# Optimization experiments

Hardware: AMD Instinct MI355X
Metric: run time of the kernel (lower is better)

## Reference

```python
import jax, jax.numpy as jnp
import numpy as np

N = 10000      # nodes
E = 80000      # edges
D = 128        # d_model
H = 8          # num_heads
DH = 128       # d_head
DFF = 512      # d_ff
CLAMP = 5.0
EPS = 1e-5


def setup_inputs() -> dict:
    key = jax.random.key(0)
    ks = jax.random.split(key, 10)
    s = 0.05
    return {
        "feat": jax.random.normal(ks[0], (N, D), jnp.float32),
        "src": jax.random.randint(ks[1], (E,), 0, N),
        "dst": jax.random.randint(ks[2], (E,), 0, N),
        # projections stored as (in, out); x @ W == torch Linear(bias=False)
        "Wq": jax.random.normal(ks[3], (D, H * DH), jnp.float32) * s,
        "Wk": jax.random.normal(ks[4], (D, H * DH), jnp.float32) * s,
        "Wv": jax.random.normal(ks[5], (D, H * DH), jnp.float32) * s,
        "Wo": jax.random.normal(ks[6], (H * DH, D), jnp.float32) * s,
        "g1": jnp.ones((D,), jnp.float32),
        "b1": jnp.zeros((D,), jnp.float32),
        "W1": jax.random.normal(ks[7], (D, DFF), jnp.float32) * s,
        "bf1": jnp.zeros((DFF,), jnp.float32),
        "W2": jax.random.normal(ks[8], (DFF, D), jnp.float32) * s,
        "bf2": jnp.zeros((D,), jnp.float32),
        "g2": jnp.ones((D,), jnp.float32),
        "b2": jnp.zeros((D,), jnp.float32),
    }


def _layer_norm(x, g, b):
    mu = x.mean(-1, keepdims=True)
    xc = x - mu
    var = (xc * xc).mean(-1, keepdims=True)
    return xc * jax.lax.rsqrt(var + EPS) * g + b


def reference(feat, src, dst, Wq, Wk, Wv, Wo, g1, b1, W1, bf1, W2, bf2, g2, b2):
    h_src = feat[src]                              # (E, D) gather
    h_dst = feat[dst]                              # (E, D)
    q = (h_dst @ Wq).reshape(E, H, DH)             # query from destination node
    k = (h_src @ Wk).reshape(E, H, DH)
    v = (h_src @ Wv).reshape(E, H, DH)
    # per-edge logits: QK dot per head, scale, clamp
    u = jnp.clip((q * k).sum(-1) / np.sqrt(DH), -CLAMP, CLAMP)  # (E, H)
    # edge_softmax over incoming edges of each destination node
    m = jax.ops.segment_max(u, dst, num_segments=N)             # (N, H)
    ex = jnp.exp(u - m[dst])
    den = jax.ops.segment_sum(ex, dst, num_segments=N)          # (N, H)
    a = ex / den[dst]                                           # (E, H)
    # weighted V, segment-sum to destination nodes
    agg = jax.ops.segment_sum(a[..., None] * v, dst, num_segments=N)  # (N, H, DH)
    uh = _layer_norm(feat + agg.reshape(N, H * DH) @ Wo, g1, b1)
    ffn = jax.nn.relu(uh @ W1 + bf1) @ W2 + bf2
    return _layer_norm(uh + ffn, g2, b2)
```

## Files before the change

kernel.cpp:

```cpp
#include <hip/hip_runtime.h>

typedef unsigned int uint;
typedef unsigned short ushort;
typedef __attribute__((ext_vector_type(8))) short short8;
typedef __attribute__((ext_vector_type(4))) float f32x4;

#define DEV static __device__ __forceinline__

DEV float bf_lo(uint v) { return __uint_as_float(v << 16); }
DEV float bf_hi(uint v) { return __uint_as_float(v & 0xffff0000u); }
DEV ushort f2bf(float f) {
    uint u = __float_as_uint(f);
    u += 0x7fffu + ((u >> 16) & 1u);
    return (ushort)(u >> 16);
}
DEV void stC(float* p, float v) { *p = v; }
DEV void stC(ushort* p, float v) { *p = f2bf(v); }

#define DPPADD(v, ctrl) \
    ((v) + __int_as_float(__builtin_amdgcn_mov_dpp(__float_as_int(v), (ctrl), 0xF, 0xF, true)))

__global__ __launch_bounds__(256) void zero_kernel(int4* __restrict__ p, int n4)
{
    int i = blockIdx.x * 256 + threadIdx.x;
    if (i < n4) p[i] = int4{0, 0, 0, 0};
}

template <typename OT>
DEV void transp_body(float (*tile)[65], const float* __restrict__ in,
                     OT* __restrict__ out, int R, int C, int bid, int t)
{
    const int nbx = C >> 6;
    const int bx = bid % nbx, by = bid / nbx;
#pragma unroll
    for (int it = 0; it < 4; ++it) {
        int idx = it * 256 + t;
        int rr = idx >> 4, cc4 = (idx & 15) * 4;
        float4 v = *reinterpret_cast<const float4*>(in + (size_t)(by * 64 + rr) * C + bx * 64 + cc4);
        tile[cc4][rr] = v.x; tile[cc4 + 1][rr] = v.y;
        tile[cc4 + 2][rr] = v.z; tile[cc4 + 3][rr] = v.w;
    }
    __syncthreads();
#pragma unroll
    for (int it = 0; it < 4; ++it) {
        int idx = it * 256 + t;
        int cc = idx >> 4, rr4 = (idx & 15) * 4;
        OT* po = out + (size_t)(bx * 64 + cc) * R + by * 64 + rr4;
        if constexpr (__is_same(OT, float)) {
            float4 o = { tile[cc][rr4], tile[cc][rr4 + 1], tile[cc][rr4 + 2], tile[cc][rr4 + 3] };
            *reinterpret_cast<float4*>(po) = o;
        } else {
            ushort4 o = { f2bf(tile[cc][rr4]), f2bf(tile[cc][rr4 + 1]),
                          f2bf(tile[cc][rr4 + 2]), f2bf(tile[cc][rr4 + 3]) };
            *reinterpret_cast<ushort4*>(po) = o;
        }
    }
}

__global__ __launch_bounds__(256) void prep0_kernel(
    const float* __restrict__ feat, ushort* __restrict__ featbf,
    const float* __restrict__ Wo, float* __restrict__ WoT,
    const float* __restrict__ W1, ushort* __restrict__ W1T,
    const float* __restrict__ W2, ushort* __restrict__ W2T,
    const int* __restrict__ dst, int* __restrict__ cntd, int N, int E)
{
    __shared__ float tile[64][65];
    const int nf = (N * 32 + 255) / 256;
    const int b = blockIdx.x, t = threadIdx.x;
    if (b < nf) {
        int i = b * 256 + t;
        if (i >= N * 32) return;
        float4 v = reinterpret_cast<const float4*>(feat)[i];
        ushort4 o;
        o.x = f2bf(v.x); o.y = f2bf(v.y); o.z = f2bf(v.z); o.w = f2bf(v.w);
        reinterpret_cast<ushort4*>(featbf)[i] = o;
    } else if (b < nf + 32) {
        transp_body<float>(tile, Wo, WoT, 1024, 128, b - nf, t);
    } else if (b < nf + 48) {
        transp_body<ushort>(tile, W1, W1T, 128, 512, b - nf - 32, t);
    } else if (b < nf + 64) {
        transp_body<ushort>(tile, W2, W2T, 512, 128, b - nf - 48, t);
    } else {
        int e = (b - nf - 64) * 256 + t;
        if (e >= E) return;
        atomicAdd(&cntd[dst[e]], 1);
    }
}

__global__ __launch_bounds__(1024) void scan1_kernel(
    const int* __restrict__ cntd, int* __restrict__ offd, int* __restrict__ curd, int N)
{
    __shared__ int ls[1024];
    const int t = threadIdx.x;
    const int chunk = (N + 1023) >> 10;
    int base = t * chunk;
    int s = 0;
    for (int i = 0; i < chunk; ++i) {
        int idx = base + i;
        if (idx < N) s += cntd[idx];
    }
    ls[t] = s;
    __syncthreads();
    for (int d = 1; d < 1024; d <<= 1) {
        int v = (t >= d) ? ls[t - d] : 0;
        __syncthreads();
        ls[t] += v;
        __syncthreads();
    }
    int run = t ? ls[t - 1] : 0;
    for (int i = 0; i < chunk; ++i) {
        int idx = base + i;
        if (idx < N) {
            offd[idx] = run;
            curd[idx] = run;
            run += cntd[idx];
        }
    }
    if (t == 1023) offd[N] = run;
}

__global__ __launch_bounds__(256) void scat_mpt_kernel(
    const int* __restrict__ src, const int* __restrict__ dst,
    int* __restrict__ curd, int* __restrict__ src_d, int* __restrict__ dst_d, int E, int eb,
    const float* __restrict__ Wq, const float* __restrict__ Wk,
    const float* __restrict__ Wv, const float* __restrict__ WoT,
    ushort* __restrict__ MPT)
{
    __shared__ char lds[65536];
    const int b = blockIdx.x, t = threadIdx.x;
    if (b < eb) {
        int e = b * 256 + t;
        if (e >= E) return;
        int s = src[e], d = dst[e];
        int pd = atomicAdd(&curd[d], 1);
        src_d[pd] = s;
        dst_d[pd] = d;
        return;
    }
    char* As = lds;
    char* Bs = lds + 32768;

    const int mb = b - eb;
    const int part = mb >> 3, h = mb & 7;
    const int lane = t & 63, w = t >> 6;
    const int frow = lane & 15, kgrp = lane >> 4;

    const float* Asrc = part ? WoT : Wk;
    const float* Bsrc = part ? Wv : Wq;
    const float ascale = part ? 1.f : 0.08838834764831845f;

#pragma unroll
    for (int it = 0; it < 16; ++it) {
        int idx = it * 256 + t;
        int r = idx >> 5, c4 = (idx & 31) * 4;
        size_t goff = (size_t)r * 1024 + h * 128 + c4;
        float4 va = *reinterpret_cast<const float4*>(Asrc + goff);
        ushort4 ua = { f2bf(va.x * ascale), f2bf(va.y * ascale),
                       f2bf(va.z * ascale), f2bf(va.w * ascale) };
        *reinterpret_cast<ushort4*>(&As[r * 256 + ((c4 * 2) ^ ((r & 7) << 4))]) = ua;
        float4 vb = *reinterpret_cast<const float4*>(Bsrc + goff);
        ushort4 ub = { f2bf(vb.x), f2bf(vb.y), f2bf(vb.z), f2bf(vb.w) };
        *reinterpret_cast<ushort4*>(&Bs[r * 256 + ((c4 * 2) ^ ((r & 7) << 4))]) = ub;
    }
    __syncthreads();

    f32x4 acc[2][8] = {};
#pragma unroll
    for (int ks = 0; ks < 4; ++ks) {
        int koff = ks * 64 + kgrp * 16;
        short8 bfr[8];
#pragma unroll
        for (int fn = 0; fn < 8; ++fn) {
            int col = fn * 16 + frow;
            bfr[fn] = *reinterpret_cast<const short8*>(&Bs[col * 256 + (koff ^ ((col & 7) << 4))]);
        }
#pragma unroll
        for (int fm = 0; fm < 2; ++fm) {
            int row = w * 32 + fm * 16 + frow;
            short8 a = *reinterpret_cast<const short8*>(&As[row * 256 + (koff ^ ((row & 7) << 4))]);
#pragma unroll
            for (int fn = 0; fn < 8; ++fn)
                acc[fm][fn] = __builtin_amdgcn_mfma_f32_16x16x32_bf16(a, bfr[fn], acc[fm][fn], 0, 0, 0);
        }
    }

    const size_t base = ((size_t)part * 1024 + h * 128) * 128;
#pragma unroll
    for (int fm = 0; fm < 2; ++fm)
#pragma unroll
        for (int fn = 0; fn < 8; ++fn)
#pragma unroll
            for (int r = 0; r < 4; ++r) {
                int j = w * 32 + fm * 16 + kgrp * 4 + r;
                int i = fn * 16 + frow;
                MPT[base + (size_t)j * 128 + i] = f2bf(acc[fm][fn][r]);
            }
}

template <int NTILE, typename OT, bool BIAS, bool RELU>
__global__ __launch_bounds__(256) void gemm_k128(
    const ushort* __restrict__ A, const ushort* __restrict__ BT,
    const float* __restrict__ bias,
    OT* __restrict__ C, int M, int NC)
{
    constexpr int FN = NTILE * 2;
    constexpr int WN = NTILE * 32;
    __shared__ char lds[32768 + NTILE * 16384];
    char* AsB = lds;
    char* BsB = lds + 32768;

    const int m0 = blockIdx.y * 128;
    const int n0 = blockIdx.x * (NTILE * 64);
    const int t = threadIdx.x;
    const int lane = t & 63, wid = t >> 6;
    const int wm = wid >> 1, wn = wid & 1;
    const int frow = lane & 15, kgrp = lane >> 4;

#pragma unroll
    for (int it = 0; it < 16; ++it) {
        int q = it * 256 + t;
        int r = q >> 4, c8 = (q & 15) * 8;
        int gm = m0 + r;
        short8 v = {};
        if (gm < M) v = *reinterpret_cast<const short8*>(&A[(size_t)gm * 128 + c8]);
        *reinterpret_cast<short8*>(&AsB[r * 256 + ((c8 * 2) ^ ((r & 7) << 4))]) = v;
    }
#pragma unroll
    for (int it = 0; it < 8 * NTILE; ++it) {
        int q = it * 256 + t;
        int r = q >> 4, c8 = (q & 15) * 8;
        short8 v = *reinterpret_cast<const short8*>(&BT[(size_t)(n0 + r) * 128 + c8]);
        *reinterpret_cast<short8*>(&BsB[r * 256 + ((c8 * 2) ^ ((r & 7) << 4))]) = v;
    }
    __syncthreads();

    f32x4 acc[4][FN] = {};
#pragma unroll
    for (int kp = 0; kp < 4; ++kp) {
        const int koff = kp * 64 + kgrp * 16;
        short8 b[FN];
#pragma unroll
        for (int fn = 0; fn < FN; ++fn) {
            int col = wn * WN + fn * 16 + frow;
            b[fn] = *reinterpret_cast<const short8*>(&BsB[col * 256 + (koff ^ ((col & 7) << 4))]);
        }
#pragma unroll
        for (int fm = 0; fm < 4; ++fm) {
            int row = wm * 64 + fm * 16 + frow;
            short8 a = *reinterpret_cast<const short8*>(&AsB[row * 256 + (koff ^ ((row & 7) << 4))]);
#pragma unroll
            for (int fn = 0; fn < FN; ++fn)
                acc[fm][fn] = __builtin_amdgcn_mfma_f32_16x16x32_bf16(a, b[fn], acc[fm][fn], 0, 0, 0);
        }
    }

#pragma unroll
    for (int fm = 0; fm < 4; ++fm)
#pragma unroll
        for (int fn = 0; fn < FN; ++fn)
#pragma unroll
            for (int r = 0; r < 4; ++r) {
                int gm = m0 + wm * 64 + fm * 16 + kgrp * 4 + r;
                int gn = n0 + wn * WN + fn * 16 + frow;
                if (gm >= M) continue;
                float v = acc[fm][fn][r];
                if (BIAS) v += bias[gn];
                if (RELU) v = fmaxf(v, 0.f);
                stC(&C[(size_t)gm * NC + gn], v);
            }
}

template <int NTILE, typename OT, bool BIAS, bool RELU, bool RES>
__global__ __launch_bounds__(256) void gemm_mfma(
    const ushort* __restrict__ A, const ushort* __restrict__ BT,
    const float* __restrict__ bias, const float* __restrict__ res,
    OT* __restrict__ C, int M, int K, int NC)
{
    constexpr int FN = NTILE * 2;
    constexpr int WN = NTILE * 32;
    __shared__ char lds[16384 + NTILE * 8192];
    char* AsB = lds;
    char* BsB = lds + 16384;

    const int m0 = blockIdx.y * 128;
    const int n0 = blockIdx.x * (NTILE * 64);
    const int t = threadIdx.x;
    const int lane = t & 63, wid = t >> 6;
    const int wm = wid >> 1, wn = wid & 1;
    const int frow = lane & 15, kgrp = lane >> 4;

    f32x4 acc[4][FN] = {};

    for (int kk = 0; kk < K; kk += 64) {
#pragma unroll
        for (int it = 0; it < 4; ++it) {
            int q = it * 256 + t;
            int r = q >> 3, c8 = (q & 7) * 8;
            int gm = m0 + r;
            short8 v = {};
            if (gm < M) v = *reinterpret_cast<const short8*>(&A[(size_t)gm * K + kk + c8]);
            *reinterpret_cast<short8*>(&AsB[r * 128 + ((c8 * 2) ^ ((r & 7) << 4))]) = v;
        }
#pragma unroll
        for (int it = 0; it < 2 * NTILE; ++it) {
            int q = it * 256 + t;
            int r = q >> 3, c8 = (q & 7) * 8;
            short8 v = *reinterpret_cast<const short8*>(&BT[(size_t)(n0 + r) * K + kk + c8]);
            *reinterpret_cast<short8*>(&BsB[r * 128 + ((c8 * 2) ^ ((r & 7) << 4))]) = v;
        }
        __syncthreads();
#pragma unroll
        for (int kp = 0; kp < 2; ++kp) {
            const int koffb = kp * 64 + kgrp * 16;
            short8 b[FN];
#pragma unroll
            for (int fn = 0; fn < FN; ++fn) {
                int col = wn * WN + fn * 16 + frow;
                b[fn] = *reinterpret_cast<const short8*>(&BsB[col * 128 + (koffb ^ ((col & 7) << 4))]);
            }
#pragma unroll
            for (int fm = 0; fm < 4; ++fm) {
                int row = wm * 64 + fm * 16 + frow;
                short8 a = *reinterpret_cast<const short8*>(&AsB[row * 128 + (koffb ^ ((row & 7) << 4))]);
#pragma unroll
                for (int fn = 0; fn < FN; ++fn)
                    acc[fm][fn] = __builtin_amdgcn_mfma_f32_16x16x32_bf16(a, b[fn], acc[fm][fn], 0, 0, 0);
            }
        }
        __syncthreads();
    }

#pragma unroll
    for (int fm = 0; fm < 4; ++fm)
#pragma unroll
        for (int fn = 0; fn < FN; ++fn)
#pragma unroll
            for (int r = 0; r < 4; ++r) {
                int gm = m0 + wm * 64 + fm * 16 + kgrp * 4 + r;
                int gn = n0 + wn * WN + fn * 16 + frow;
                if (gm >= M) continue;
                float v = acc[fm][fn][r];
                if (BIAS) v += bias[gn];
                if (RELU) v = fmaxf(v, 0.f);
                if (RES) v += res[(size_t)gm * NC + gn];
                stC(&C[(size_t)gm * NC + gn], v);
            }
}

__global__ __launch_bounds__(256) void edge_logits2_kernel(
    const ushort* __restrict__ featbf, const ushort* __restrict__ GVO,
    const int* __restrict__ src_d, const int* __restrict__ dst_d,
    float* __restrict__ exws, int E)
{
    int w = (int)((blockIdx.x * 256 + threadIdx.x) >> 6);
    int lane = threadIdx.x & 63;
    int el = lane >> 4, li = lane & 15;
    int p = w * 4 + el;
    if (p >= E) return;
    int s = src_d[p], d = dst_d[p];
    uint4 f = reinterpret_cast<const uint4*>(featbf)[(size_t)s * 16 + li];
    const uint4* Grow = reinterpret_cast<const uint4*>(GVO) + (size_t)d * 256 + li;
    float sel = 0.f;
#pragma unroll
    for (int h = 0; h < 8; ++h) {
        uint4 g = Grow[h * 16];
        float pv = bf_lo(g.x) * bf_lo(f.x) + bf_hi(g.x) * bf_hi(f.x);
        pv += bf_lo(g.y) * bf_lo(f.y) + bf_hi(g.y) * bf_hi(f.y);
        pv += bf_lo(g.z) * bf_lo(f.z) + bf_hi(g.z) * bf_hi(f.z);
        pv += bf_lo(g.w) * bf_lo(f.w) + bf_hi(g.w) * bf_hi(f.w);
        pv = DPPADD(pv, 0xB1);
        pv = DPPADD(pv, 0x4E);
        pv = DPPADD(pv, 0x141);
        pv = DPPADD(pv, 0x128);
        sel = (li == h) ? pv : sel;
    }
    float u = fminf(fmaxf(sel, -5.f), 5.f);
    float ex = __expf(u);
    if (li < 8) exws[(size_t)p * 8 + li] = ex;
}

__global__ __launch_bounds__(256) void aggden_ln1_kernel(
    const ushort* __restrict__ GVO, const int* __restrict__ src_d,
    const int* __restrict__ offd, const float* __restrict__ exws,
    const float* __restrict__ feat, const float* __restrict__ g1,
    const float* __restrict__ b1, float* __restrict__ uh,
    ushort* __restrict__ uhbf, int N)
{
    int d = (int)((blockIdx.x * 256 + threadIdx.x) >> 6);
    int lane = threadIdx.x & 63;
    if (d >= N) return;
    const int lo = offd[d], hi = offd[d + 1];

    int h = lane & 7;
    float den = 0.f;
    for (int i = lo + (lane >> 3); i < hi; i += 8)
        den += exws[(size_t)i * 8 + h];
    den += __shfl_xor(den, 8);
    den += __shfl_xor(den, 16);
    den += __shfl_xor(den, 32);
    float rh = 1.f / den;
    float rv0 = __shfl(rh, 0), rv1 = __shfl(rh, 1), rv2 = __shfl(rh, 2), rv3 = __shfl(rh, 3);
    float rv4 = __shfl(rh, 4), rv5 = __shfl(rh, 5), rv6 = __shfl(rh, 6), rv7 = __shfl(rh, 7);

    float acc0 = 0.f, acc1 = 0.f;
    int snext = (lo < hi) ? src_d[lo] : 0;
    for (int i = lo; i < hi; ++i) {
        int s = snext;
        if (i + 1 < hi) snext = src_d[i + 1];
        float4 e0 = *reinterpret_cast<const float4*>(&exws[(size_t)i * 8]);
        float4 e1 = *reinterpret_cast<const float4*>(&exws[(size_t)i * 8 + 4]);
        const uint* vrow = reinterpret_cast<const uint*>(GVO + (size_t)s * 2048 + 1024);
        uint gv0 = vrow[0 * 64 + lane], gv1 = vrow[1 * 64 + lane];
        uint gv2 = vrow[2 * 64 + lane], gv3 = vrow[3 * 64 + lane];
        uint gv4 = vrow[4 * 64 + lane], gv5 = vrow[5 * 64 + lane];
        uint gv6 = vrow[6 * 64 + lane], gv7 = vrow[7 * 64 + lane];
        float a0 = e0.x * rv0, a1 = e0.y * rv1, a2 = e0.z * rv2, a3 = e0.w * rv3;
        float a4 = e1.x * rv4, a5 = e1.y * rv5, a6 = e1.z * rv6, a7 = e1.w * rv7;
        acc0 += a0 * bf_lo(gv0) + a1 * bf_lo(gv1) + a2 * bf_lo(gv2) + a3 * bf_lo(gv3)
              + a4 * bf_lo(gv4) + a5 * bf_lo(gv5) + a6 * bf_lo(gv6) + a7 * bf_lo(gv7);
        acc1 += a0 * bf_hi(gv0) + a1 * bf_hi(gv1) + a2 * bf_hi(gv2) + a3 * bf_hi(gv3)
              + a4 * bf_hi(gv4) + a5 * bf_hi(gv5) + a6 * bf_hi(gv6) + a7 * bf_hi(gv7);
    }

    float2 v = reinterpret_cast<const float2*>(feat)[(size_t)d * 64 + lane];
    v.x += acc0;
    v.y += acc1;
    float sum = v.x + v.y;
#pragma unroll
    for (int off = 32; off; off >>= 1) sum += __shfl_xor(sum, off);
    float mean = sum * (1.f / 128.f);
    float cx = v.x - mean, cy = v.y - mean;
    float vs = cx * cx + cy * cy;
#pragma unroll
    for (int off = 32; off; off >>= 1) vs += __shfl_xor(vs, off);
    float r = rsqrtf(vs * (1.f / 128.f) + 1e-5f);
    float2 gg = reinterpret_cast<const float2*>(g1)[lane];
    float2 bb = reinterpret_cast<const float2*>(b1)[lane];
    float2 o;
    o.x = cx * r * gg.x + bb.x;
    o.y = cy * r * gg.y + bb.y;
    reinterpret_cast<float2*>(uh)[(size_t)d * 64 + lane] = o;
    ushort2 ob; ob.x = f2bf(o.x); ob.y = f2bf(o.y);
    reinterpret_cast<ushort2*>(uhbf)[(size_t)d * 64 + lane] = ob;
}

__global__ __launch_bounds__(256) void ln_kernel(
    const float* __restrict__ x, const float* __restrict__ g,
    const float* __restrict__ b, float* __restrict__ out, int M)
{
    int row = (int)((blockIdx.x * 256 + threadIdx.x) >> 6);
    int lane = threadIdx.x & 63;
    if (row >= M) return;
    float2 v = reinterpret_cast<const float2*>(x)[(size_t)row * 64 + lane];
    float sum = v.x + v.y;
#pragma unroll
    for (int off = 32; off; off >>= 1) sum += __shfl_xor(sum, off);
    float mean = sum * (1.f / 128.f);
    float cx = v.x - mean, cy = v.y - mean;
    float vs = cx * cx + cy * cy;
#pragma unroll
    for (int off = 32; off; off >>= 1) vs += __shfl_xor(vs, off);
    float r = rsqrtf(vs * (1.f / 128.f) + 1e-5f);
    float2 gg = reinterpret_cast<const float2*>(g)[lane];
    float2 bb = reinterpret_cast<const float2*>(b)[lane];
    float2 o;
    o.x = cx * r * gg.x + bb.x;
    o.y = cy * r * gg.y + bb.y;
    reinterpret_cast<float2*>(out)[(size_t)row * 64 + lane] = o;
}

extern "C" void kernel_launch(void* const* d_in, const int* in_sizes, int n_in,
                              void* d_out, int out_size, void* d_ws, size_t ws_size,
                              hipStream_t stream)
{
    const float* feat = (const float*)d_in[0];
    const int*   src  = (const int*)d_in[1];
    const int*   dst  = (const int*)d_in[2];
    const float* Wq   = (const float*)d_in[3];
    const float* Wk   = (const float*)d_in[4];
    const float* Wv   = (const float*)d_in[5];
    const float* Wo   = (const float*)d_in[6];
    const float* g1   = (const float*)d_in[7];
    const float* b1   = (const float*)d_in[8];
    const float* W1   = (const float*)d_in[9];
    const float* bf1  = (const float*)d_in[10];
    const float* W2   = (const float*)d_in[11];
    const float* bf2  = (const float*)d_in[12];
    const float* g2   = (const float*)d_in[13];
    const float* b2   = (const float*)d_in[14];
    const int N = in_sizes[0] / 128;
    const int E = in_sizes[1];
    float* out = (float*)d_out;

    char* w = (char*)d_ws;
    auto alloc = [&](size_t bytes) {
        char* p = w;
        w += (bytes + 255) & ~(size_t)255;
        return p;
    };
    ushort* MPT    = (ushort*)alloc((size_t)2048 * 128 * 2);
    float*  WoT    = (float*)alloc((size_t)128 * 1024 * 4);
    ushort* W1T    = (ushort*)alloc((size_t)512 * 128 * 2);
    ushort* W2T    = (ushort*)alloc((size_t)128 * 512 * 2);
    ushort* featbf = (ushort*)alloc((size_t)N * 128 * 2);
    ushort* GVO    = (ushort*)alloc((size_t)N * 2048 * 2);
    float*  exws   = (float*)alloc((size_t)E * 8 * 4);
    int*    cntd   = (int*)alloc((size_t)((N + 3) & ~3) * 4);
    int*    offd   = (int*)alloc((size_t)(N + 1) * 4);
    int*    curd   = (int*)alloc((size_t)N * 4);
    int*    src_d  = (int*)alloc((size_t)E * 4);
    int*    dst_d  = (int*)alloc((size_t)E * 4);
    float*  uh     = (float*)alloc((size_t)N * 128 * 4);
    ushort* uhbf   = (ushort*)alloc((size_t)N * 128 * 2);
    ushort* f1     = (ushort*)alloc((size_t)N * 512 * 2);
    float*  pre2   = (float*)alloc((size_t)N * 128 * 4);

    int n4 = (N + 3) / 4;
    zero_kernel<<<(n4 + 255) / 256, 256, 0, stream>>>((int4*)cntd, n4);

    int nf = (N * 32 + 255) / 256;
    int eb = (E + 255) / 256;
    prep0_kernel<<<nf + 64 + eb, 256, 0, stream>>>(
        feat, featbf, Wo, WoT, W1, W1T, W2, W2T, dst, cntd, N, E);

    scan1_kernel<<<1, 1024, 0, stream>>>(cntd, offd, curd, N);
    scat_mpt_kernel<<<eb + 16, 256, 0, stream>>>(
        src, dst, curd, src_d, dst_d, E, eb, Wq, Wk, Wv, WoT, MPT);

    dim3 gv_grid(2048 / 128, (N + 127) / 128);
    gemm_k128<2, ushort, false, false><<<gv_grid, 256, 0, stream>>>(
        featbf, MPT, nullptr, GVO, N, 2048);

    edge_logits2_kernel<<<(E + 15) / 16, 256, 0, stream>>>(featbf, GVO, src_d, dst_d, exws, E);
    int nwaves_n = (N * 64 + 255) / 256;
    aggden_ln1_kernel<<<nwaves_n, 256, 0, stream>>>(
        GVO, src_d, offd, exws, feat, g1, b1, uh, uhbf, N);

    dim3 f1_grid(512 / 128, (N + 127) / 128);
    gemm_k128<2, ushort, true, true><<<f1_grid, 256, 0, stream>>>(
        uhbf, W1T, bf1, f1, N, 512);
    dim3 f2_grid(128 / 64, (N + 127) / 128);
    gemm_mfma<1, float, true, false, true><<<f2_grid, 256, 0, stream>>>(
        f1, W2T, bf2, uh, pre2, N, 512, 128);

    ln_kernel<<<nwaves_n, 256, 0, stream>>>(pre2, g2, b2, out, N);
}
```

Measured before the change: 149.0 us.

## Split histogram from prep, use K-looped GEMM for K=128, add 64x64 FFN2 GEMM

Folds the count-zeroing into the prep kernel and moves the dst histogram atomics into their own kernel. The single-shot K=128 GEMM (which staged all of K in LDS) is replaced by the generic K-looped gemm_mfma for the GV and FFN1 projections. A new 64x64-tile GEMM handles FFN2 (K=512, N=128), doubling the block count so more CUs get work. The trade-off is smaller tiles with less reuse per block, plus one extra kernel launch for the histogram.

Measured after the change: 127.6 us. 1.17x faster.

```diff
diff --git a/kernel.cpp b/kernel.cpp
--- a/kernel.cpp
+++ b/kernel.cpp
@@ -19,12 +19,6 @@
 
 #define DPPADD(v, ctrl) \
     ((v) + __int_as_float(__builtin_amdgcn_mov_dpp(__float_as_int(v), (ctrl), 0xF, 0xF, true)))
-
-__global__ __launch_bounds__(256) void zero_kernel(int4* __restrict__ p, int n4)
-{
-    int i = blockIdx.x * 256 + threadIdx.x;
-    if (i < n4) p[i] = int4{0, 0, 0, 0};
-}
 
 template <typename OT>
 DEV void transp_body(float (*tile)[65], const float* __restrict__ in,
@@ -57,34 +51,42 @@
     }
 }
 
-__global__ __launch_bounds__(256) void prep0_kernel(
+__global__ __launch_bounds__(256) void prep1_kernel(
+    int4* __restrict__ cntd4, int nz,
     const float* __restrict__ feat, ushort* __restrict__ featbf,
     const float* __restrict__ Wo, float* __restrict__ WoT,
     const float* __restrict__ W1, ushort* __restrict__ W1T,
-    const float* __restrict__ W2, ushort* __restrict__ W2T,
-    const int* __restrict__ dst, int* __restrict__ cntd, int N, int E)
+    const float* __restrict__ W2, ushort* __restrict__ W2T, int N)
 {
     __shared__ float tile[64][65];
+    const int zb = (nz + 255) / 256;
     const int nf = (N * 32 + 255) / 256;
     const int b = blockIdx.x, t = threadIdx.x;
-    if (b < nf) {
+    if (b < zb) {
         int i = b * 256 + t;
+        if (i < nz) cntd4[i] = int4{0, 0, 0, 0};
+    } else if (b < zb + nf) {
+        int i = (b - zb) * 256 + t;
         if (i >= N * 32) return;
         float4 v = reinterpret_cast<const float4*>(feat)[i];
         ushort4 o;
         o.x = f2bf(v.x); o.y = f2bf(v.y); o.z = f2bf(v.z); o.w = f2bf(v.w);
         reinterpret_cast<ushort4*>(featbf)[i] = o;
-    } else if (b < nf + 32) {
-        transp_body<float>(tile, Wo, WoT, 1024, 128, b - nf, t);
-    } else if (b < nf + 48) {
-        transp_body<ushort>(tile, W1, W1T, 128, 512, b - nf - 32, t);
-    } else if (b < nf + 64) {
-        transp_body<ushort>(tile, W2, W2T, 512, 128, b - nf - 48, t);
+    } else if (b < zb + nf + 32) {
+        transp_body<float>(tile, Wo, WoT, 1024, 128, b - zb - nf, t);
+    } else if (b < zb + nf + 48) {
+        transp_body<ushort>(tile, W1, W1T, 128, 512, b - zb - nf - 32, t);
     } else {
-        int e = (b - nf - 64) * 256 + t;
-        if (e >= E) return;
-        atomicAdd(&cntd[dst[e]], 1);
-    }
+        transp_body<ushort>(tile, W2, W2T, 512, 128, b - zb - nf - 48, t);
+    }
+}
+
+__global__ __launch_bounds__(256) void hist_kernel(
+    const int* __restrict__ dst, int* __restrict__ cntd, int E)
+{
+    int e = blockIdx.x * 256 + threadIdx.x;
+    if (e >= E) return;
+    atomicAdd(&cntd[dst[e]], 1);
 }
 
 __global__ __launch_bounds__(1024) void scan1_kernel(
@@ -197,79 +199,6 @@
             }
 }
 
-template <int NTILE, typename OT, bool BIAS, bool RELU>
-__global__ __launch_bounds__(256) void gemm_k128(
-    const ushort* __restrict__ A, const ushort* __restrict__ BT,
-    const float* __restrict__ bias,
-    OT* __restrict__ C, int M, int NC)
-{
-    constexpr int FN = NTILE * 2;
-    constexpr int WN = NTILE * 32;
-    __shared__ char lds[32768 + NTILE * 16384];
-    char* AsB = lds;
-    char* BsB = lds + 32768;
-
-    const int m0 = blockIdx.y * 128;
-    const int n0 = blockIdx.x * (NTILE * 64);
-    const int t = threadIdx.x;
-    const int lane = t & 63, wid = t >> 6;
-    const int wm = wid >> 1, wn = wid & 1;
-    const int frow = lane & 15, kgrp = lane >> 4;
-
-#pragma unroll
-    for (int it = 0; it < 16; ++it) {
-        int q = it * 256 + t;
-        int r = q >> 4, c8 = (q & 15) * 8;
-        int gm = m0 + r;
-        short8 v = {};
-        if (gm < M) v = *reinterpret_cast<const short8*>(&A[(size_t)gm * 128 + c8]);
-        *reinterpret_cast<short8*>(&AsB[r * 256 + ((c8 * 2) ^ ((r & 7) << 4))]) = v;
-    }
-#pragma unroll
-    for (int it = 0; it < 8 * NTILE; ++it) {
-        int q = it * 256 + t;
-        int r = q >> 4, c8 = (q & 15) * 8;
-        short8 v = *reinterpret_cast<const short8*>(&BT[(size_t)(n0 + r) * 128 + c8]);
-        *reinterpret_cast<short8*>(&BsB[r * 256 + ((c8 * 2) ^ ((r & 7) << 4))]) = v;
-    }
-    __syncthreads();
-
-    f32x4 acc[4][FN] = {};
-#pragma unroll
-    for (int kp = 0; kp < 4; ++kp) {
-        const int koff = kp * 64 + kgrp * 16;
-        short8 b[FN];
-#pragma unroll
-        for (int fn = 0; fn < FN; ++fn) {
-            int col = wn * WN + fn * 16 + frow;
-            b[fn] = *reinterpret_cast<const short8*>(&BsB[col * 256 + (koff ^ ((col & 7) << 4))]);
-        }
-#pragma unroll
-        for (int fm = 0; fm < 4; ++fm) {
-            int row = wm * 64 + fm * 16 + frow;
-            short8 a = *reinterpret_cast<const short8*>(&AsB[row * 256 + (koff ^ ((row & 7) << 4))]);
-#pragma unroll
-            for (int fn = 0; fn < FN; ++fn)
-                acc[fm][fn] = __builtin_amdgcn_mfma_f32_16x16x32_bf16(a, b[fn], acc[fm][fn], 0, 0, 0);
-        }
-    }
-
-#pragma unroll
-    for (int fm = 0; fm < 4; ++fm)
-#pragma unroll
-        for (int fn = 0; fn < FN; ++fn)
-#pragma unroll
-            for (int r = 0; r < 4; ++r) {
-                int gm = m0 + wm * 64 + fm * 16 + kgrp * 4 + r;
-                int gn = n0 + wn * WN + fn * 16 + frow;
-                if (gm >= M) continue;
-                float v = acc[fm][fn][r];
-                if (BIAS) v += bias[gn];
-                if (RELU) v = fmaxf(v, 0.f);
-                stC(&C[(size_t)gm * NC + gn], v);
-            }
-}
-
 template <int NTILE, typename OT, bool BIAS, bool RELU, bool RES>
 __global__ __launch_bounds__(256) void gemm_mfma(
     const ushort* __restrict__ A, const ushort* __restrict__ BT,
@@ -344,6 +273,77 @@
                 if (RELU) v = fmaxf(v, 0.f);
                 if (RES) v += res[(size_t)gm * NC + gn];
                 stC(&C[(size_t)gm * NC + gn], v);
+            }
+}
+
+__global__ __launch_bounds__(256) void gemm_mfma64(
+    const ushort* __restrict__ A, const ushort* __restrict__ BT,
+    const float* __restrict__ bias, const float* __restrict__ res,
+    float* __restrict__ C, int M, int K, int NC)
+{
+    __shared__ char lds[16384];
+    char* AsB = lds;
+    char* BsB = lds + 8192;
+
+    const int m0 = blockIdx.y * 64;
+    const int n0 = blockIdx.x * 64;
+    const int t = threadIdx.x;
+    const int lane = t & 63, wid = t >> 6;
+    const int wm = wid >> 1, wn = wid & 1;
+    const int frow = lane & 15, kgrp = lane >> 4;
+
+    f32x4 acc[2][2] = {};
+
+    for (int kk = 0; kk < K; kk += 64) {
+#pragma unroll
+        for (int it = 0; it < 2; ++it) {
+            int q = it * 256 + t;
+            int r = q >> 3, c8 = (q & 7) * 8;
+            int gm = m0 + r;
+            short8 v = {};
+            if (gm < M) v = *reinterpret_cast<const short8*>(&A[(size_t)gm * K + kk + c8]);
+            *reinterpret_cast<short8*>(&AsB[r * 128 + ((c8 * 2) ^ ((r & 7) << 4))]) = v;
+        }
+#pragma unroll
+        for (int it = 0; it < 2; ++it) {
+            int q = it * 256 + t;
+            int r = q >> 3, c8 = (q & 7) * 8;
+            short8 v = *reinterpret_cast<const short8*>(&BT[(size_t)(n0 + r) * K + kk + c8]);
+            *reinterpret_cast<short8*>(&BsB[r * 128 + ((c8 * 2) ^ ((r & 7) << 4))]) = v;
+        }
+        __syncthreads();
+#pragma unroll
+        for (int kp = 0; kp < 2; ++kp) {
+            const int koffb = kp * 64 + kgrp * 16;
+            short8 b[2];
+#pragma unroll
+            for (int fn = 0; fn < 2; ++fn) {
+                int col = wn * 32 + fn * 16 + frow;
+                b[fn] = *reinterpret_cast<const short8*>(&BsB[col * 128 + (koffb ^ ((col & 7) << 4))]);
+            }
+#pragma unroll
+            for (int fm = 0; fm < 2; ++fm) {
+                int row = wm * 32 + fm * 16 + frow;
+                short8 a = *reinterpret_cast<const short8*>(&AsB[row * 128 + (koffb ^ ((row & 7) << 4))]);
+#pragma unroll
+                for (int fn = 0; fn < 2; ++fn)
+                    acc[fm][fn] = __builtin_amdgcn_mfma_f32_16x16x32_bf16(a, b[fn], acc[fm][fn], 0, 0, 0);
+            }
+        }
+        __syncthreads();
+    }
+
+#pragma unroll
+    for (int fm = 0; fm < 2; ++fm)
+#pragma unroll
+        for (int fn = 0; fn < 2; ++fn)
+#pragma unroll
+            for (int r = 0; r < 4; ++r) {
+                int gm = m0 + wm * 32 + fm * 16 + kgrp * 4 + r;
+                int gn = n0 + wn * 32 + fn * 16 + frow;
+                if (gm >= M) continue;
+                float v = acc[fm][fn][r] + bias[gn] + res[(size_t)gm * NC + gn];
+                C[(size_t)gm * NC + gn] = v;
             }
 }
 
@@ -515,21 +515,21 @@
     ushort* f1     = (ushort*)alloc((size_t)N * 512 * 2);
     float*  pre2   = (float*)alloc((size_t)N * 128 * 4);
 
-    int n4 = (N + 3) / 4;
-    zero_kernel<<<(n4 + 255) / 256, 256, 0, stream>>>((int4*)cntd, n4);
-
+    int nz = (N + 3) / 4;
+    int zb = (nz + 255) / 256;
     int nf = (N * 32 + 255) / 256;
+    prep1_kernel<<<zb + nf + 64, 256, 0, stream>>>(
+        (int4*)cntd, nz, feat, featbf, Wo, WoT, W1, W1T, W2, W2T, N);
+
     int eb = (E + 255) / 256;
-    prep0_kernel<<<nf + 64 + eb, 256, 0, stream>>>(
-        feat, featbf, Wo, WoT, W1, W1T, W2, W2T, dst, cntd, N, E);
-
+    hist_kernel<<<eb, 256, 0, stream>>>(dst, cntd, E);
     scan1_kernel<<<1, 1024, 0, stream>>>(cntd, offd, curd, N);
     scat_mpt_kernel<<<eb + 16, 256, 0, stream>>>(
         src, dst, curd, src_d, dst_d, E, eb, Wq, Wk, Wv, WoT, MPT);
 
     dim3 gv_grid(2048 / 128, (N + 127) / 128);
-    gemm_k128<2, ushort, false, false><<<gv_grid, 256, 0, stream>>>(
-        featbf, MPT, nullptr, GVO, N, 2048);
+    gemm_mfma<2, ushort, false, false, false><<<gv_grid, 256, 0, stream>>>(
+        featbf, MPT, nullptr, nullptr, GVO, N, 128, 2048);
 
     edge_logits2_kernel<<<(E + 15) / 16, 256, 0, stream>>>(featbf, GVO, src_d, dst_d, exws, E);
     int nwaves_n = (N * 64 + 255) / 256;
@@ -537,10 +537,10 @@
         GVO, src_d, offd, exws, feat, g1, b1, uh, uhbf, N);
 
     dim3 f1_grid(512 / 128, (N + 127) / 128);
-    gemm_k128<2, ushort, true, true><<<f1_grid, 256, 0, stream>>>(
-        uhbf, W1T, bf1, f1, N, 512);
-    dim3 f2_grid(128 / 64, (N + 127) / 128);
-    gemm_mfma<1, float, true, false, true><<<f2_grid, 256, 0, stream>>>(
+    gemm_mfma<2, ushort, true, true, false><<<f1_grid, 256, 0, stream>>>(
+        uhbf, W1T, bf1, nullptr, f1, N, 128, 512);
+    dim3 f2_grid(128 / 64, (N + 63) / 64);
+    gemm_mfma64<<<f2_grid, 256, 0, stream>>>(
         f1, W2T, bf2, uh, pre2, N, 512, 128);
 
     ln_kernel<<<nwaves_n, 256, 0, stream>>>(pre2, g2, b2, out, N);
```
